# Performance work log

Measured on AMD Instinct MI355X. Metric: run time of the kernel, lower is better.

The kernel has to match this reference:

```python
import jax, jax.numpy as jnp
import numpy as np

B, H, V, S = 64, 1024, 32000, 128


def setup_inputs() -> dict:
    key = jax.random.key(0)
    ks = jax.random.split(key, 16)
    s = 1.0 / np.sqrt(H)
    return {
        "prev_input": jax.random.randint(ks[0], (B,), 0, V),
        "h0": jax.random.normal(ks[1], (B, H), jnp.float32),
        "c0": jax.random.normal(ks[2], (B, H), jnp.float32),
        "encoder_outputs": jax.random.normal(ks[3], (B, H, S), jnp.float32),
        "emb": jax.random.normal(ks[4], (V, H), jnp.float32),
        "W_ih": jax.random.uniform(ks[5], (4 * H, H), jnp.float32, -s, s),
        "W_hh": jax.random.uniform(ks[6], (4 * H, H), jnp.float32, -s, s),
        "b_ih": jax.random.uniform(ks[7], (4 * H,), jnp.float32, -s, s),
        "b_hh": jax.random.uniform(ks[8], (4 * H,), jnp.float32, -s, s),
        "W1_w": jax.random.uniform(ks[9], (H, H), jnp.float32, -s, s),
        "W1_b": jax.random.uniform(ks[10], (H,), jnp.float32, -s, s),
        "W2_w": jax.random.uniform(ks[11], (H, H), jnp.float32, -s, s),
        "W2_b": jax.random.uniform(ks[12], (H,), jnp.float32, -s, s),
        "W_w": jax.random.uniform(ks[13], (V, H), jnp.float32, -s, s),
        "W_b": jax.random.uniform(ks[14], (V,), jnp.float32, -s, s),
    }


def reference(prev_input, h0, c0, encoder_outputs, emb, W_ih, W_hh, b_ih, b_hh,
              W1_w, W1_b, W2_w, W2_b, W_w, W_b):
    # Embedding lookup (dropout omitted: eval mode)
    x = emb[prev_input]  # (B, H)
    # Single LSTM step (PyTorch gate order: i, f, g, o)
    gates = x @ W_ih.T + b_ih + h0 @ W_hh.T + b_hh  # (B, 4H)
    i, f, g, o = jnp.split(gates, 4, axis=-1)
    c_new = jax.nn.sigmoid(f) * c0 + jax.nn.sigmoid(i) * jnp.tanh(g)
    h_new = jax.nn.sigmoid(o) * jnp.tanh(c_new)  # (B, H)
    # Bahdanau-style dot attention over encoder_outputs (B, H, S)
    alpha = jax.nn.softmax(jnp.einsum('bh,bhs->bs', h_new, encoder_outputs), axis=-1)
    t = jnp.einsum('bs,bhs->bh', alpha, encoder_outputs)  # (B, H)
    # MLP classifier head
    h_att = jnp.tanh(h_new @ W1_w.T + W1_b + t @ W2_w.T + W2_b)
    y = h_att @ W_w.T + W_b  # (B, V)
    pred = jax.nn.log_softmax(y, axis=-1)
    return (pred, h_new, c_new)
```

## Files before the change

kernel.cpp:

```cpp
#include <hip/hip_runtime.h>
#include <hip/hip_bf16.h>
#include <cstdint>
#include <cstddef>

#define B_ 64
#define H_ 1024
#define V_ 32000
#define S_ 128

#define WS_GATES   0
#define WS_SCORE   524288
#define WS_HATTP   589824
#define WS_Y       851968
#define WS_BF      2899968

#define OUT_H      2048000
#define OUT_C      2113536

typedef __attribute__((ext_vector_type(8))) short bf16x8;
typedef __attribute__((ext_vector_type(4))) float f32x4;

__device__ __forceinline__ void bsplit(float x, unsigned short& hi, unsigned short& lo) {
  const unsigned int xb = __float_as_uint(x);
  hi = (unsigned short)(xb >> 16);
  const float r = x - __uint_as_float(xb & 0xFFFF0000u);
  lo = (unsigned short)(__float_as_uint(r) >> 16);
}

__global__ __launch_bounds__(256) void prep_split(
    const int* __restrict__ prev, const float* __restrict__ emb,
    const float* __restrict__ h0,
    unsigned short* __restrict__ xhi, unsigned short* __restrict__ xlo,
    unsigned short* __restrict__ hhi, unsigned short* __restrict__ hlo)
{
  const int b = blockIdx.x;
  const int k4 = threadIdx.x * 4;
  const float4 xv = *reinterpret_cast<const float4*>(emb + (size_t)prev[b] * H_ + k4);
  const float4 hv = *reinterpret_cast<const float4*>(h0 + (size_t)b * H_ + k4);
  ushort4 a, c, d, e;
  bsplit(xv.x, a.x, c.x); bsplit(xv.y, a.y, c.y);
  bsplit(xv.z, a.z, c.z); bsplit(xv.w, a.w, c.w);
  bsplit(hv.x, d.x, e.x); bsplit(hv.y, d.y, e.y);
  bsplit(hv.z, d.z, e.z); bsplit(hv.w, d.w, e.w);
  const size_t o = (size_t)b * H_ + k4;
  *reinterpret_cast<ushort4*>(xhi + o) = a;
  *reinterpret_cast<ushort4*>(xlo + o) = c;
  *reinterpret_cast<ushort4*>(hhi + o) = d;
  *reinterpret_cast<ushort4*>(hlo + o) = e;
}

__global__ __launch_bounds__(128) void gates_mfma(
    const unsigned short* __restrict__ xhi, const unsigned short* __restrict__ xlo,
    const unsigned short* __restrict__ hhi, const unsigned short* __restrict__ hlo,
    const float* __restrict__ W_ih, const float* __restrict__ W_hh,
    float* __restrict__ gates_part)
{
  const int tid = threadIdx.x;
  const int wave = tid >> 6, lane = tid & 63;
  const int l15 = lane & 15, lk = lane >> 4;
  const int ks = blockIdx.y;
  const int n = blockIdx.x * 32 + wave * 16 + l15;
  const float* W = ks ? W_hh : W_ih;
  const unsigned short* Ah = ks ? hhi : xhi;
  const unsigned short* Al = ks ? hlo : xlo;
  const float* wp = W + (size_t)n * H_ + lk * 8;
  const unsigned short* ah_base = Ah + l15 * H_ + lk * 8;
  const unsigned short* al_base = Al + l15 * H_ + lk * 8;

  f32x4 acc[4];
  #pragma unroll
  for (int mt = 0; mt < 4; ++mt) acc[mt] = (f32x4){0.f, 0.f, 0.f, 0.f};

  #pragma unroll 2
  for (int c = 0; c < 32; ++c) {
    const int k0 = c * 32;
    const float4 wv0 = *reinterpret_cast<const float4*>(wp + k0);
    const float4 wv1 = *reinterpret_cast<const float4*>(wp + k0 + 4);
    const float wf[8] = {wv0.x, wv0.y, wv0.z, wv0.w, wv1.x, wv1.y, wv1.z, wv1.w};
    bf16x8 whi, wlo;
    #pragma unroll
    for (int e = 0; e < 8; ++e) {
      const unsigned int xb = __float_as_uint(wf[e]);
      whi[e] = (short)(xb >> 16);
      const float lof = wf[e] - __uint_as_float(xb & 0xFFFF0000u);
      wlo[e] = (short)(__float_as_uint(lof) >> 16);
    }
    #pragma unroll
    for (int mt = 0; mt < 4; ++mt) {
      const bf16x8 ah = *reinterpret_cast<const bf16x8*>(ah_base + (size_t)mt * 16 * H_ + k0);
      const bf16x8 al = *reinterpret_cast<const bf16x8*>(al_base + (size_t)mt * 16 * H_ + k0);
      acc[mt] = __builtin_amdgcn_mfma_f32_16x16x32_bf16(ah, whi, acc[mt], 0, 0, 0);
      acc[mt] = __builtin_amdgcn_mfma_f32_16x16x32_bf16(al, whi, acc[mt], 0, 0, 0);
      acc[mt] = __builtin_amdgcn_mfma_f32_16x16x32_bf16(ah, wlo, acc[mt], 0, 0, 0);
    }
  }
  #pragma unroll
  for (int mt = 0; mt < 4; ++mt)
    #pragma unroll
    for (int r = 0; r < 4; ++r)
      gates_part[((size_t)ks * 64 + mt * 16 + lk * 4 + r) * 4096 + n] = acc[mt][r];
}

__global__ __launch_bounds__(128) void lstm_scores(
    const float* __restrict__ gates_part,
    const float* __restrict__ b_ih, const float* __restrict__ b_hh,
    const float* __restrict__ c0, const float* __restrict__ enc,
    float* __restrict__ out_h, float* __restrict__ out_c,
    unsigned short* __restrict__ hnhi, unsigned short* __restrict__ hnlo,
    float* __restrict__ score_part)
{
  __shared__ float hs[128];
  const int b = blockIdx.x >> 3, hc = blockIdx.x & 7;
  const int tid = threadIdx.x;
  const int h = hc * 128 + tid;

  float gi = b_ih[h]        + b_hh[h];
  float gf = b_ih[1024 + h] + b_hh[1024 + h];
  float gg = b_ih[2048 + h] + b_hh[2048 + h];
  float go = b_ih[3072 + h] + b_hh[3072 + h];
  #pragma unroll
  for (int ks = 0; ks < 2; ++ks) {
    const float* g = gates_part + ((size_t)ks * 64 + b) * 4096;
    gi += g[h]; gf += g[1024 + h]; gg += g[2048 + h]; go += g[3072 + h];
  }
  const float si = 1.f / (1.f + expf(-gi));
  const float sf = 1.f / (1.f + expf(-gf));
  const float so = 1.f / (1.f + expf(-go));
  const float cn = sf * c0[b * H_ + h] + si * tanhf(gg);
  const float hn = so * tanhf(cn);
  out_c[b * H_ + h] = cn;
  out_h[b * H_ + h] = hn;
  unsigned short hi_, lo_;
  bsplit(hn, hi_, lo_);
  hnhi[b * H_ + h] = hi_;
  hnlo[b * H_ + h] = lo_;
  hs[tid] = hn;
  __syncthreads();

  const float* e = enc + ((size_t)b * H_ + hc * 128) * S_ + tid;
  float acc = 0.f;
  #pragma unroll 8
  for (int j = 0; j < 128; ++j) acc += hs[j] * e[(size_t)j * S_];
  score_part[((size_t)hc * 64 + b) * S_ + tid] = acc;
}

__global__ __launch_bounds__(256) void attn_ctx(
    const float* __restrict__ score_part, const float* __restrict__ enc,
    unsigned short* __restrict__ thi, unsigned short* __restrict__ tlo)
{
  __shared__ __align__(16) float al[128];
  __shared__ float red[4];
  const int b = blockIdx.x >> 3, hg = blockIdx.x & 7;
  const int tid = threadIdx.x;

  float sc = 0.f;
  if (tid < 128) {
    #pragma unroll
    for (int ks = 0; ks < 8; ++ks) sc += score_part[((size_t)ks * 64 + b) * S_ + tid];
  }
  float v = (tid < 128) ? sc : -3.4e38f;
  #pragma unroll
  for (int off = 32; off; off >>= 1) v = fmaxf(v, __shfl_xor(v, off));
  if (tid == 0)  red[0] = v;
  if (tid == 64) red[1] = v;
  __syncthreads();
  const float mx = fmaxf(red[0], red[1]);
  const float ex = (tid < 128) ? expf(sc - mx) : 0.f;
  float sv = ex;
  #pragma unroll
  for (int off = 32; off; off >>= 1) sv += __shfl_xor(sv, off);
  if (tid == 0)  red[2] = sv;
  if (tid == 64) red[3] = sv;
  __syncthreads();
  const float inv = 1.f / (red[2] + red[3]);
  if (tid < 128) al[tid] = ex * inv;
  __syncthreads();

  const int wave = tid >> 6, lane = tid & 63;
  const int hoff = lane >> 5, s4 = (lane & 31) * 4;
  const float4 av = *reinterpret_cast<const float4*>(&al[s4]);
  const int hbase = hg * 128 + wave * 32;
  #pragma unroll 4
  for (int r = 0; r < 16; ++r) {
    const int h = hbase + r * 2 + hoff;
    const float4 ev = *reinterpret_cast<const float4*>(enc + ((size_t)b * H_ + h) * S_ + s4);
    float acc = ev.x * av.x + ev.y * av.y + ev.z * av.z + ev.w * av.w;
    #pragma unroll
    for (int off = 16; off; off >>= 1) acc += __shfl_xor(acc, off);
    if ((lane & 31) == 0) {
      unsigned short hi_, lo_;
      bsplit(acc, hi_, lo_);
      thi[b * H_ + h] = hi_;
      tlo[b * H_ + h] = lo_;
    }
  }
}

__global__ __launch_bounds__(128) void hatt_mfma(
    const unsigned short* __restrict__ hnhi, const unsigned short* __restrict__ hnlo,
    const unsigned short* __restrict__ thi, const unsigned short* __restrict__ tlo,
    const float* __restrict__ W1, const float* __restrict__ W2,
    float* __restrict__ hatt_part)
{
  const int tid = threadIdx.x;
  const int wave = tid >> 6, lane = tid & 63;
  const int l15 = lane & 15, lk = lane >> 4;
  const int ks = blockIdx.y;
  const int n = blockIdx.x * 32 + wave * 16 + l15;
  const int koff = (ks & 1) * 512;
  const float* W = (ks < 2) ? W1 : W2;
  const unsigned short* Ah = (ks < 2) ? hnhi : thi;
  const unsigned short* Al = (ks < 2) ? hnlo : tlo;
  const float* wp = W + (size_t)n * H_ + koff + lk * 8;
  const unsigned short* ah_base = Ah + l15 * H_ + koff + lk * 8;
  const unsigned short* al_base = Al + l15 * H_ + koff + lk * 8;

  f32x4 acc[4];
  #pragma unroll
  for (int mt = 0; mt < 4; ++mt) acc[mt] = (f32x4){0.f, 0.f, 0.f, 0.f};

  #pragma unroll 2
  for (int c = 0; c < 16; ++c) {
    const int k0 = c * 32;
    const float4 wv0 = *reinterpret_cast<const float4*>(wp + k0);
    const float4 wv1 = *reinterpret_cast<const float4*>(wp + k0 + 4);
    const float wf[8] = {wv0.x, wv0.y, wv0.z, wv0.w, wv1.x, wv1.y, wv1.z, wv1.w};
    bf16x8 whi, wlo;
    #pragma unroll
    for (int e = 0; e < 8; ++e) {
      const unsigned int xb = __float_as_uint(wf[e]);
      whi[e] = (short)(xb >> 16);
      const float lof = wf[e] - __uint_as_float(xb & 0xFFFF0000u);
      wlo[e] = (short)(__float_as_uint(lof) >> 16);
    }
    #pragma unroll
    for (int mt = 0; mt < 4; ++mt) {
      const bf16x8 ah = *reinterpret_cast<const bf16x8*>(ah_base + (size_t)mt * 16 * H_ + k0);
      const bf16x8 al = *reinterpret_cast<const bf16x8*>(al_base + (size_t)mt * 16 * H_ + k0);
      acc[mt] = __builtin_amdgcn_mfma_f32_16x16x32_bf16(ah, whi, acc[mt], 0, 0, 0);
      acc[mt] = __builtin_amdgcn_mfma_f32_16x16x32_bf16(al, whi, acc[mt], 0, 0, 0);
      acc[mt] = __builtin_amdgcn_mfma_f32_16x16x32_bf16(ah, wlo, acc[mt], 0, 0, 0);
    }
  }
  #pragma unroll
  for (int mt = 0; mt < 4; ++mt)
    #pragma unroll
    for (int r = 0; r < 4; ++r)
      hatt_part[((size_t)ks * 64 + mt * 16 + lk * 4 + r) * 1024 + n] = acc[mt][r];
}

__global__ __launch_bounds__(256) void hatt_ep(
    const float* __restrict__ hatt_part,
    const float* __restrict__ b1, const float* __restrict__ b2,
    unsigned short* __restrict__ Ahi, unsigned short* __restrict__ Alo)
{
  const int i = blockIdx.x * 256 + threadIdx.x;
  const int col = i & (H_ - 1);
  float a = b1[col] + b2[col];
  #pragma unroll
  for (int ks = 0; ks < 4; ++ks) a += hatt_part[(size_t)ks * 65536 + i];
  const float t = tanhf(a);
  unsigned short hi_, lo_;
  bsplit(t, hi_, lo_);
  Ahi[i] = hi_;
  Alo[i] = lo_;
}

__global__ __launch_bounds__(256, 2) void gemm_big_mfma(
    const unsigned short* __restrict__ Ahi, const unsigned short* __restrict__ Alo,
    const float* __restrict__ W, const float* __restrict__ bias,
    float* __restrict__ y)
{
  const int tid = threadIdx.x;
  const int wave = tid >> 6, lane = tid & 63;
  const int l15 = lane & 15, lk = lane >> 4;
  const int n = blockIdx.x * 64 + wave * 16 + l15;
  const float* wp = W + (size_t)n * H_ + lk * 8;
  const unsigned short* ah_base = Ahi + l15 * H_ + lk * 8;
  const unsigned short* al_base = Alo + l15 * H_ + lk * 8;

  f32x4 acc[4];
  #pragma unroll
  for (int mt = 0; mt < 4; ++mt) acc[mt] = (f32x4){0.f, 0.f, 0.f, 0.f};

  #pragma unroll 4
  for (int ks = 0; ks < 32; ++ks) {
    const int k0 = ks * 32;
    const float4 wv0 = *reinterpret_cast<const float4*>(wp + k0);
    const float4 wv1 = *reinterpret_cast<const float4*>(wp + k0 + 4);
    const float wf[8] = {wv0.x, wv0.y, wv0.z, wv0.w, wv1.x, wv1.y, wv1.z, wv1.w};
    bf16x8 whi, wlo;
    #pragma unroll
    for (int e = 0; e < 8; ++e) {
      const unsigned int xb = __float_as_uint(wf[e]);
      whi[e] = (short)(xb >> 16);
      const float lof = wf[e] - __uint_as_float(xb & 0xFFFF0000u);
      wlo[e] = (short)(__float_as_uint(lof) >> 16);
    }
    #pragma unroll
    for (int mt = 0; mt < 4; ++mt) {
      const bf16x8 ah = *reinterpret_cast<const bf16x8*>(ah_base + (size_t)mt * 16 * H_ + k0);
      const bf16x8 al = *reinterpret_cast<const bf16x8*>(al_base + (size_t)mt * 16 * H_ + k0);
      acc[mt] = __builtin_amdgcn_mfma_f32_16x16x32_bf16(ah, whi, acc[mt], 0, 0, 0);
      acc[mt] = __builtin_amdgcn_mfma_f32_16x16x32_bf16(al, whi, acc[mt], 0, 0, 0);
      acc[mt] = __builtin_amdgcn_mfma_f32_16x16x32_bf16(ah, wlo, acc[mt], 0, 0, 0);
    }
  }
  const float bn = bias[n];
  #pragma unroll
  for (int mt = 0; mt < 4; ++mt)
    #pragma unroll
    for (int r = 0; r < 4; ++r)
      y[(size_t)(mt * 16 + lk * 4 + r) * V_ + n] = acc[mt][r] + bn;
}

__global__ __launch_bounds__(1024) void lse_pred(
    const float* __restrict__ y, float* __restrict__ pred)
{
  __shared__ float red[16];
  __shared__ float bc;
  const int b = blockIdx.x, tid = threadIdx.x;
  const float* yr = y + (size_t)b * V_;

  float m = -3.4e38f;
  for (int i = tid; i < V_; i += 1024) m = fmaxf(m, yr[i]);
  #pragma unroll
  for (int off = 32; off; off >>= 1) m = fmaxf(m, __shfl_xor(m, off));
  if ((tid & 63) == 0) red[tid >> 6] = m;
  __syncthreads();
  if (tid == 0) {
    float mx = red[0];
    #pragma unroll
    for (int w = 1; w < 16; ++w) mx = fmaxf(mx, red[w]);
    bc = mx;
  }
  __syncthreads();
  const float mx = bc;
  float s = 0.f;
  for (int i = tid; i < V_; i += 1024) s += expf(yr[i] - mx);
  #pragma unroll
  for (int off = 32; off; off >>= 1) s += __shfl_xor(s, off);
  if ((tid & 63) == 0) red[tid >> 6] = s;
  __syncthreads();
  if (tid == 0) {
    float tot = 0.f;
    #pragma unroll
    for (int w = 0; w < 16; ++w) tot += red[w];
    bc = mx + logf(tot);
  }
  __syncthreads();
  const float lse = bc;
  float* pr = pred + (size_t)b * V_;
  for (int i = tid; i < V_; i += 1024) pr[i] = yr[i] - lse;
}

extern "C" void kernel_launch(void* const* d_in, const int* in_sizes, int n_in,
                              void* d_out, int out_size, void* d_ws, size_t ws_size,
                              hipStream_t stream)
{
  const int*   prev = (const int*)  d_in[0];
  const float* h0   = (const float*)d_in[1];
  const float* c0   = (const float*)d_in[2];
  const float* enc  = (const float*)d_in[3];
  const float* emb  = (const float*)d_in[4];
  const float* W_ih = (const float*)d_in[5];
  const float* W_hh = (const float*)d_in[6];
  const float* b_ih = (const float*)d_in[7];
  const float* b_hh = (const float*)d_in[8];
  const float* W1_w = (const float*)d_in[9];
  const float* W1_b = (const float*)d_in[10];
  const float* W2_w = (const float*)d_in[11];
  const float* W2_b = (const float*)d_in[12];
  const float* W_w  = (const float*)d_in[13];
  const float* W_b  = (const float*)d_in[14];

  float* outp  = (float*)d_out;
  float* pred  = outp;
  float* h_new = outp + OUT_H;
  float* c_new = outp + OUT_C;

  float* ws         = (float*)d_ws;
  float* gates_part = ws + WS_GATES;
  float* score_part = ws + WS_SCORE;
  float* hatt_part  = ws + WS_HATTP;
  float* y          = ws + WS_Y;
  unsigned short* us = (unsigned short*)(ws + WS_BF);
  unsigned short* xhi  = us;
  unsigned short* xlo  = us + 65536;
  unsigned short* h0hi = us + 131072;
  unsigned short* h0lo = us + 196608;
  unsigned short* hnhi = us + 262144;
  unsigned short* hnlo = us + 327680;
  unsigned short* thi  = us + 393216;
  unsigned short* tlo  = us + 458752;
  unsigned short* Ahi  = us + 524288;
  unsigned short* Alo  = us + 589824;

  prep_split<<<64, 256, 0, stream>>>(prev, emb, h0, xhi, xlo, h0hi, h0lo);
  gates_mfma<<<dim3(128, 2), 128, 0, stream>>>(
      xhi, xlo, h0hi, h0lo, W_ih, W_hh, gates_part);
  lstm_scores<<<512, 128, 0, stream>>>(
      gates_part, b_ih, b_hh, c0, enc, h_new, c_new, hnhi, hnlo, score_part);
  attn_ctx<<<512, 256, 0, stream>>>(score_part, enc, thi, tlo);
  hatt_mfma<<<dim3(32, 4), 128, 0, stream>>>(
      hnhi, hnlo, thi, tlo, W1_w, W2_w, hatt_part);
  hatt_ep<<<256, 256, 0, stream>>>(hatt_part, W1_b, W2_b, Ahi, Alo);
  gemm_big_mfma<<<500, 256, 0, stream>>>(Ahi, Alo, W_w, W_b, y);
  lse_pred<<<64, 1024, 0, stream>>>(y, pred);
}
```

Measured before the change: 419.6 us.

## Split-K all GEMMs, software-pipeline weight loads, split LSTM/scores and two-pass log-softmax

```diff
diff --git a/kernel.cpp b/kernel.cpp
--- a/kernel.cpp
+++ b/kernel.cpp
@@ -9,10 +9,11 @@
 #define S_ 128
 
 #define WS_GATES   0
-#define WS_SCORE   524288
-#define WS_HATTP   589824
-#define WS_Y       851968
-#define WS_BF      2899968
+#define WS_SCORE   2097152
+#define WS_HATTP   2228224
+#define WS_YP      2752512
+#define WS_STATS   6848512
+#define WS_BF      6849536
 
 #define OUT_H      2048000
 #define OUT_C      2113536
@@ -25,6 +26,48 @@
   hi = (unsigned short)(xb >> 16);
   const float r = x - __uint_as_float(xb & 0xFFFF0000u);
   lo = (unsigned short)(__float_as_uint(r) >> 16);
+}
+
+template<int NITER>
+__device__ __forceinline__ void mfma_panel(
+    const float* __restrict__ wp,
+    const unsigned short* __restrict__ ah_base,
+    const unsigned short* __restrict__ al_base,
+    f32x4 acc[4])
+{
+  float4 w0 = *reinterpret_cast<const float4*>(wp);
+  float4 w1 = *reinterpret_cast<const float4*>(wp + 4);
+  #pragma unroll
+  for (int c = 0; c < NITER; ++c) {
+    const int k0 = c * 32;
+    float4 nw0, nw1;
+    if (c + 1 < NITER) {
+      nw0 = *reinterpret_cast<const float4*>(wp + k0 + 32);
+      nw1 = *reinterpret_cast<const float4*>(wp + k0 + 36);
+    }
+    bf16x8 ah[4], al[4];
+    #pragma unroll
+    for (int mt = 0; mt < 4; ++mt) {
+      ah[mt] = *reinterpret_cast<const bf16x8*>(ah_base + (size_t)mt * 16 * H_ + k0);
+      al[mt] = *reinterpret_cast<const bf16x8*>(al_base + (size_t)mt * 16 * H_ + k0);
+    }
+    const float wf[8] = {w0.x, w0.y, w0.z, w0.w, w1.x, w1.y, w1.z, w1.w};
+    bf16x8 whi, wlo;
+    #pragma unroll
+    for (int e = 0; e < 8; ++e) {
+      const unsigned int xb = __float_as_uint(wf[e]);
+      whi[e] = (short)(xb >> 16);
+      const float lof = wf[e] - __uint_as_float(xb & 0xFFFF0000u);
+      wlo[e] = (short)(__float_as_uint(lof) >> 16);
+    }
+    #pragma unroll
+    for (int mt = 0; mt < 4; ++mt) {
+      acc[mt] = __builtin_amdgcn_mfma_f32_16x16x32_bf16(ah[mt], whi, acc[mt], 0, 0, 0);
+      acc[mt] = __builtin_amdgcn_mfma_f32_16x16x32_bf16(al[mt], whi, acc[mt], 0, 0, 0);
+      acc[mt] = __builtin_amdgcn_mfma_f32_16x16x32_bf16(ah[mt], wlo, acc[mt], 0, 0, 0);
+    }
+    if (c + 1 < NITER) { w0 = nw0; w1 = nw1; }
+  }
 }
 
 __global__ __launch_bounds__(256) void prep_split(
@@ -49,7 +92,7 @@
   *reinterpret_cast<ushort4*>(hlo + o) = e;
 }
 
-__global__ __launch_bounds__(128) void gates_mfma(
+__global__ __launch_bounds__(256, 4) void gates_mfma(
     const unsigned short* __restrict__ xhi, const unsigned short* __restrict__ xlo,
     const unsigned short* __restrict__ hhi, const unsigned short* __restrict__ hlo,
     const float* __restrict__ W_ih, const float* __restrict__ W_hh,
@@ -59,41 +102,18 @@
   const int wave = tid >> 6, lane = tid & 63;
   const int l15 = lane & 15, lk = lane >> 4;
   const int ks = blockIdx.y;
-  const int n = blockIdx.x * 32 + wave * 16 + l15;
-  const float* W = ks ? W_hh : W_ih;
-  const unsigned short* Ah = ks ? hhi : xhi;
-  const unsigned short* Al = ks ? hlo : xlo;
-  const float* wp = W + (size_t)n * H_ + lk * 8;
-  const unsigned short* ah_base = Ah + l15 * H_ + lk * 8;
-  const unsigned short* al_base = Al + l15 * H_ + lk * 8;
+  const int mat = ks >> 2, koff = (ks & 3) * 256;
+  const int n = blockIdx.x * 64 + wave * 16 + l15;
+  const float* W = mat ? W_hh : W_ih;
+  const unsigned short* Ah = mat ? hhi : xhi;
+  const unsigned short* Al = mat ? hlo : xlo;
 
   f32x4 acc[4];
   #pragma unroll
   for (int mt = 0; mt < 4; ++mt) acc[mt] = (f32x4){0.f, 0.f, 0.f, 0.f};
-
-  #pragma unroll 2
-  for (int c = 0; c < 32; ++c) {
-    const int k0 = c * 32;
-    const float4 wv0 = *reinterpret_cast<const float4*>(wp + k0);
-    const float4 wv1 = *reinterpret_cast<const float4*>(wp + k0 + 4);
-    const float wf[8] = {wv0.x, wv0.y, wv0.z, wv0.w, wv1.x, wv1.y, wv1.z, wv1.w};
-    bf16x8 whi, wlo;
-    #pragma unroll
-    for (int e = 0; e < 8; ++e) {
-      const unsigned int xb = __float_as_uint(wf[e]);
-      whi[e] = (short)(xb >> 16);
-      const float lof = wf[e] - __uint_as_float(xb & 0xFFFF0000u);
-      wlo[e] = (short)(__float_as_uint(lof) >> 16);
-    }
-    #pragma unroll
-    for (int mt = 0; mt < 4; ++mt) {
-      const bf16x8 ah = *reinterpret_cast<const bf16x8*>(ah_base + (size_t)mt * 16 * H_ + k0);
-      const bf16x8 al = *reinterpret_cast<const bf16x8*>(al_base + (size_t)mt * 16 * H_ + k0);
-      acc[mt] = __builtin_amdgcn_mfma_f32_16x16x32_bf16(ah, whi, acc[mt], 0, 0, 0);
-      acc[mt] = __builtin_amdgcn_mfma_f32_16x16x32_bf16(al, whi, acc[mt], 0, 0, 0);
-      acc[mt] = __builtin_amdgcn_mfma_f32_16x16x32_bf16(ah, wlo, acc[mt], 0, 0, 0);
-    }
-  }
+  mfma_panel<8>(W + (size_t)n * H_ + koff + lk * 8,
+                Ah + l15 * H_ + koff + lk * 8,
+                Al + l15 * H_ + koff + lk * 8, acc);
   #pragma unroll
   for (int mt = 0; mt < 4; ++mt)
     #pragma unroll
@@ -101,46 +121,51 @@
       gates_part[((size_t)ks * 64 + mt * 16 + lk * 4 + r) * 4096 + n] = acc[mt][r];
 }
 
-__global__ __launch_bounds__(128) void lstm_scores(
+__global__ __launch_bounds__(256) void k_lstm(
     const float* __restrict__ gates_part,
     const float* __restrict__ b_ih, const float* __restrict__ b_hh,
-    const float* __restrict__ c0, const float* __restrict__ enc,
+    const float* __restrict__ c0,
     float* __restrict__ out_h, float* __restrict__ out_c,
-    unsigned short* __restrict__ hnhi, unsigned short* __restrict__ hnlo,
-    float* __restrict__ score_part)
-{
-  __shared__ float hs[128];
-  const int b = blockIdx.x >> 3, hc = blockIdx.x & 7;
-  const int tid = threadIdx.x;
-  const int h = hc * 128 + tid;
-
+    unsigned short* __restrict__ hnhi, unsigned short* __restrict__ hnlo)
+{
+  const int i = blockIdx.x * 256 + threadIdx.x;
+  const int h = i & (H_ - 1);
   float gi = b_ih[h]        + b_hh[h];
   float gf = b_ih[1024 + h] + b_hh[1024 + h];
   float gg = b_ih[2048 + h] + b_hh[2048 + h];
   float go = b_ih[3072 + h] + b_hh[3072 + h];
-  #pragma unroll
-  for (int ks = 0; ks < 2; ++ks) {
+  const int b = i >> 10;
+  #pragma unroll
+  for (int ks = 0; ks < 8; ++ks) {
     const float* g = gates_part + ((size_t)ks * 64 + b) * 4096;
     gi += g[h]; gf += g[1024 + h]; gg += g[2048 + h]; go += g[3072 + h];
   }
   const float si = 1.f / (1.f + expf(-gi));
   const float sf = 1.f / (1.f + expf(-gf));
   const float so = 1.f / (1.f + expf(-go));
-  const float cn = sf * c0[b * H_ + h] + si * tanhf(gg);
+  const float cn = sf * c0[i] + si * tanhf(gg);
   const float hn = so * tanhf(cn);
-  out_c[b * H_ + h] = cn;
-  out_h[b * H_ + h] = hn;
+  out_c[i] = cn;
+  out_h[i] = hn;
   unsigned short hi_, lo_;
   bsplit(hn, hi_, lo_);
-  hnhi[b * H_ + h] = hi_;
-  hnlo[b * H_ + h] = lo_;
-  hs[tid] = hn;
+  hnhi[i] = hi_;
+  hnlo[i] = lo_;
+}
+
+__global__ __launch_bounds__(128) void k_scores(
+    const float* __restrict__ h_new, const float* __restrict__ enc,
+    float* __restrict__ score_part)
+{
+  __shared__ float hs[64];
+  const int b = blockIdx.x >> 4, hc = blockIdx.x & 15;
+  const int tid = threadIdx.x;
+  if (tid < 64) hs[tid] = h_new[b * H_ + hc * 64 + tid];
   __syncthreads();
-
-  const float* e = enc + ((size_t)b * H_ + hc * 128) * S_ + tid;
+  const float* e = enc + ((size_t)b * H_ + hc * 64) * S_ + tid;
   float acc = 0.f;
   #pragma unroll 8
-  for (int j = 0; j < 128; ++j) acc += hs[j] * e[(size_t)j * S_];
+  for (int j = 0; j < 64; ++j) acc += hs[j] * e[(size_t)j * S_];
   score_part[((size_t)hc * 64 + b) * S_ + tid] = acc;
 }
 
@@ -156,7 +181,7 @@
   float sc = 0.f;
   if (tid < 128) {
     #pragma unroll
-    for (int ks = 0; ks < 8; ++ks) sc += score_part[((size_t)ks * 64 + b) * S_ + tid];
+    for (int ks = 0; ks < 16; ++ks) sc += score_part[((size_t)ks * 64 + b) * S_ + tid];
   }
   float v = (tid < 128) ? sc : -3.4e38f;
   #pragma unroll
@@ -180,7 +205,7 @@
   const int hoff = lane >> 5, s4 = (lane & 31) * 4;
   const float4 av = *reinterpret_cast<const float4*>(&al[s4]);
   const int hbase = hg * 128 + wave * 32;
-  #pragma unroll 4
+  #pragma unroll 8
   for (int r = 0; r < 16; ++r) {
     const int h = hbase + r * 2 + hoff;
     const float4 ev = *reinterpret_cast<const float4*>(enc + ((size_t)b * H_ + h) * S_ + s4);
@@ -196,7 +221,7 @@
   }
 }
 
-__global__ __launch_bounds__(128) void hatt_mfma(
+__global__ __launch_bounds__(256, 4) void hatt_mfma(
     const unsigned short* __restrict__ hnhi, const unsigned short* __restrict__ hnlo,
     const unsigned short* __restrict__ thi, const unsigned short* __restrict__ tlo,
     const float* __restrict__ W1, const float* __restrict__ W2,
@@ -206,42 +231,18 @@
   const int wave = tid >> 6, lane = tid & 63;
   const int l15 = lane & 15, lk = lane >> 4;
   const int ks = blockIdx.y;
-  const int n = blockIdx.x * 32 + wave * 16 + l15;
-  const int koff = (ks & 1) * 512;
-  const float* W = (ks < 2) ? W1 : W2;
-  const unsigned short* Ah = (ks < 2) ? hnhi : thi;
-  const unsigned short* Al = (ks < 2) ? hnlo : tlo;
-  const float* wp = W + (size_t)n * H_ + koff + lk * 8;
-  const unsigned short* ah_base = Ah + l15 * H_ + koff + lk * 8;
-  const unsigned short* al_base = Al + l15 * H_ + koff + lk * 8;
+  const int mat = ks >> 2, koff = (ks & 3) * 256;
+  const int n = blockIdx.x * 64 + wave * 16 + l15;
+  const float* W = mat ? W2 : W1;
+  const unsigned short* Ah = mat ? thi : hnhi;
+  const unsigned short* Al = mat ? tlo : hnlo;
 
   f32x4 acc[4];
   #pragma unroll
   for (int mt = 0; mt < 4; ++mt) acc[mt] = (f32x4){0.f, 0.f, 0.f, 0.f};
-
-  #pragma unroll 2
-  for (int c = 0; c < 16; ++c) {
-    const int k0 = c * 32;
-    const float4 wv0 = *reinterpret_cast<const float4*>(wp + k0);
-    const float4 wv1 = *reinterpret_cast<const float4*>(wp + k0 + 4);
-    const float wf[8] = {wv0.x, wv0.y, wv0.z, wv0.w, wv1.x, wv1.y, wv1.z, wv1.w};
-    bf16x8 whi, wlo;
-    #pragma unroll
-    for (int e = 0; e < 8; ++e) {
-      const unsigned int xb = __float_as_uint(wf[e]);
-      whi[e] = (short)(xb >> 16);
-      const float lof = wf[e] - __uint_as_float(xb & 0xFFFF0000u);
-      wlo[e] = (short)(__float_as_uint(lof) >> 16);
-    }
-    #pragma unroll
-    for (int mt = 0; mt < 4; ++mt) {
-      const bf16x8 ah = *reinterpret_cast<const bf16x8*>(ah_base + (size_t)mt * 16 * H_ + k0);
-      const bf16x8 al = *reinterpret_cast<const bf16x8*>(al_base + (size_t)mt * 16 * H_ + k0);
-      acc[mt] = __builtin_amdgcn_mfma_f32_16x16x32_bf16(ah, whi, acc[mt], 0, 0, 0);
-      acc[mt] = __builtin_amdgcn_mfma_f32_16x16x32_bf16(al, whi, acc[mt], 0, 0, 0);
-      acc[mt] = __builtin_amdgcn_mfma_f32_16x16x32_bf16(ah, wlo, acc[mt], 0, 0, 0);
-    }
-  }
+  mfma_panel<8>(W + (size_t)n * H_ + koff + lk * 8,
+                Ah + l15 * H_ + koff + lk * 8,
+                Al + l15 * H_ + koff + lk * 8, acc);
   #pragma unroll
   for (int mt = 0; mt < 4; ++mt)
     #pragma unroll
@@ -258,7 +259,7 @@
   const int col = i & (H_ - 1);
   float a = b1[col] + b2[col];
   #pragma unroll
-  for (int ks = 0; ks < 4; ++ks) a += hatt_part[(size_t)ks * 65536 + i];
+  for (int ks = 0; ks < 8; ++ks) a += hatt_part[(size_t)ks * 65536 + i];
   const float t = tanhf(a);
   unsigned short hi_, lo_;
   bsplit(t, hi_, lo_);
@@ -266,92 +267,101 @@
   Alo[i] = lo_;
 }
 
-__global__ __launch_bounds__(256, 2) void gemm_big_mfma(
+__global__ __launch_bounds__(256, 4) void gemm_big_mfma(
     const unsigned short* __restrict__ Ahi, const unsigned short* __restrict__ Alo,
-    const float* __restrict__ W, const float* __restrict__ bias,
-    float* __restrict__ y)
+    const float* __restrict__ W, float* __restrict__ ypart)
 {
   const int tid = threadIdx.x;
   const int wave = tid >> 6, lane = tid & 63;
   const int l15 = lane & 15, lk = lane >> 4;
+  const int ks = blockIdx.y, koff = ks * 512;
   const int n = blockIdx.x * 64 + wave * 16 + l15;
-  const float* wp = W + (size_t)n * H_ + lk * 8;
-  const unsigned short* ah_base = Ahi + l15 * H_ + lk * 8;
-  const unsigned short* al_base = Alo + l15 * H_ + lk * 8;
 
   f32x4 acc[4];
   #pragma unroll
   for (int mt = 0; mt < 4; ++mt) acc[mt] = (f32x4){0.f, 0.f, 0.f, 0.f};
-
-  #pragma unroll 4
-  for (int ks = 0; ks < 32; ++ks) {
-    const int k0 = ks * 32;
-    const float4 wv0 = *reinterpret_cast<const float4*>(wp + k0);
-    const float4 wv1 = *reinterpret_cast<const float4*>(wp + k0 + 4);
-    const float wf[8] = {wv0.x, wv0.y, wv0.z, wv0.w, wv1.x, wv1.y, wv1.z, wv1.w};
-    bf16x8 whi, wlo;
-    #pragma unroll
-    for (int e = 0; e < 8; ++e) {
-      const unsigned int xb = __float_as_uint(wf[e]);
-      whi[e] = (short)(xb >> 16);
-      const float lof = wf[e] - __uint_as_float(xb & 0xFFFF0000u);
-      wlo[e] = (short)(__float_as_uint(lof) >> 16);
-    }
-    #pragma unroll
-    for (int mt = 0; mt < 4; ++mt) {
-      const bf16x8 ah = *reinterpret_cast<const bf16x8*>(ah_base + (size_t)mt * 16 * H_ + k0);
-      const bf16x8 al = *reinterpret_cast<const bf16x8*>(al_base + (size_t)mt * 16 * H_ + k0);
-      acc[mt] = __builtin_amdgcn_mfma_f32_16x16x32_bf16(ah, whi, acc[mt], 0, 0, 0);
-      acc[mt] = __builtin_amdgcn_mfma_f32_16x16x32_bf16(al, whi, acc[mt], 0, 0, 0);
-      acc[mt] = __builtin_amdgcn_mfma_f32_16x16x32_bf16(ah, wlo, acc[mt], 0, 0, 0);
-    }
-  }
-  const float bn = bias[n];
+  mfma_panel<16>(W + (size_t)n * H_ + koff + lk * 8,
+                 Ahi + l15 * H_ + koff + lk * 8,
+                 Alo + l15 * H_ + koff + lk * 8, acc);
+  float* yp = ypart + (size_t)ks * 64 * V_;
   #pragma unroll
   for (int mt = 0; mt < 4; ++mt)
     #pragma unroll
     for (int r = 0; r < 4; ++r)
-      y[(size_t)(mt * 16 + lk * 4 + r) * V_ + n] = acc[mt][r] + bn;
-}
-
-__global__ __launch_bounds__(1024) void lse_pred(
-    const float* __restrict__ y, float* __restrict__ pred)
-{
-  __shared__ float red[16];
-  __shared__ float bc;
-  const int b = blockIdx.x, tid = threadIdx.x;
-  const float* yr = y + (size_t)b * V_;
-
+      yp[(size_t)(mt * 16 + lk * 4 + r) * V_ + n] = acc[mt][r];
+}
+
+__global__ __launch_bounds__(256) void lse1(
+    const float* __restrict__ yp, const float* __restrict__ bias,
+    float* __restrict__ stats)
+{
+  __shared__ float sm[4][2];
+  const int b = blockIdx.x >> 3, ch = blockIdx.x & 7;
+  const int tid = threadIdx.x;
+  const float* p0 = yp + (size_t)b * V_ + ch * 4000;
+  const float* p1 = p0 + (size_t)64 * V_;
+  const float* bs = bias + ch * 4000;
+
+  float v[16];
   float m = -3.4e38f;
-  for (int i = tid; i < V_; i += 1024) m = fmaxf(m, yr[i]);
-  #pragma unroll
-  for (int off = 32; off; off >>= 1) m = fmaxf(m, __shfl_xor(m, off));
-  if ((tid & 63) == 0) red[tid >> 6] = m;
+  #pragma unroll
+  for (int j = 0; j < 16; ++j) {
+    const int c = tid + j * 256;
+    if (c < 4000) {
+      v[j] = p0[c] + p1[c] + bs[c];
+      m = fmaxf(m, v[j]);
+    }
+  }
+  float s = 0.f;
+  #pragma unroll
+  for (int j = 0; j < 16; ++j) {
+    const int c = tid + j * 256;
+    if (c < 4000) s += expf(v[j] - m);
+  }
+  #pragma unroll
+  for (int off = 32; off; off >>= 1) {
+    const float m2 = __shfl_xor(m, off);
+    const float s2 = __shfl_xor(s, off);
+    const float M = fmaxf(m, m2);
+    s = s * expf(m - M) + s2 * expf(m2 - M);
+    m = M;
+  }
+  if ((tid & 63) == 0) { sm[tid >> 6][0] = m; sm[tid >> 6][1] = s; }
   __syncthreads();
   if (tid == 0) {
-    float mx = red[0];
-    #pragma unroll
-    for (int w = 1; w < 16; ++w) mx = fmaxf(mx, red[w]);
-    bc = mx;
-  }
-  __syncthreads();
-  const float mx = bc;
-  float s = 0.f;
-  for (int i = tid; i < V_; i += 1024) s += expf(yr[i] - mx);
-  #pragma unroll
-  for (int off = 32; off; off >>= 1) s += __shfl_xor(s, off);
-  if ((tid & 63) == 0) red[tid >> 6] = s;
-  __syncthreads();
-  if (tid == 0) {
-    float tot = 0.f;
-    #pragma unroll
-    for (int w = 0; w < 16; ++w) tot += red[w];
-    bc = mx + logf(tot);
-  }
-  __syncthreads();
-  const float lse = bc;
-  float* pr = pred + (size_t)b * V_;
-  for (int i = tid; i < V_; i += 1024) pr[i] = yr[i] - lse;
+    float M = fmaxf(fmaxf(sm[0][0], sm[1][0]), fmaxf(sm[2][0], sm[3][0]));
+    float S = 0.f;
+    #pragma unroll
+    for (int w = 0; w < 4; ++w) S += sm[w][1] * expf(sm[w][0] - M);
+    stats[(b * 8 + ch) * 2]     = M;
+    stats[(b * 8 + ch) * 2 + 1] = S;
+  }
+}
+
+__global__ __launch_bounds__(256) void lse2(
+    const float* __restrict__ yp, const float* __restrict__ bias,
+    const float* __restrict__ stats, float* __restrict__ pred)
+{
+  const int b = blockIdx.x >> 3, ch = blockIdx.x & 7;
+  const int tid = threadIdx.x;
+  float M = -3.4e38f;
+  #pragma unroll
+  for (int i = 0; i < 8; ++i) M = fmaxf(M, stats[(b * 8 + i) * 2]);
+  float S = 0.f;
+  #pragma unroll
+  for (int i = 0; i < 8; ++i)
+    S += stats[(b * 8 + i) * 2 + 1] * expf(stats[(b * 8 + i) * 2] - M);
+  const float lse = M + logf(S);
+
+  const float* p0 = yp + (size_t)b * V_ + ch * 4000;
+  const float* p1 = p0 + (size_t)64 * V_;
+  const float* bs = bias + ch * 4000;
+  float* pr = pred + (size_t)b * V_ + ch * 4000;
+  #pragma unroll
+  for (int j = 0; j < 16; ++j) {
+    const int c = tid + j * 256;
+    if (c < 4000) pr[c] = p0[c] + p1[c] + bs[c] - lse;
+  }
 }
 
 extern "C" void kernel_launch(void* const* d_in, const int* in_sizes, int n_in,
@@ -383,7 +393,8 @@
   float* gates_part = ws + WS_GATES;
   float* score_part = ws + WS_SCORE;
   float* hatt_part  = ws + WS_HATTP;
-  float* y          = ws + WS_Y;
+  float* ypart      = ws + WS_YP;
+  float* stats      = ws + WS_STATS;
   unsigned short* us = (unsigned short*)(ws + WS_BF);
   unsigned short* xhi  = us;
   unsigned short* xlo  = us + 65536;
@@ -397,14 +408,16 @@
   unsigned short* Alo  = us + 589824;
 
   prep_split<<<64, 256, 0, stream>>>(prev, emb, h0, xhi, xlo, h0hi, h0lo);
-  gates_mfma<<<dim3(128, 2), 128, 0, stream>>>(
+  gates_mfma<<<dim3(64, 8), 256, 0, stream>>>(
       xhi, xlo, h0hi, h0lo, W_ih, W_hh, gates_part);
-  lstm_scores<<<512, 128, 0, stream>>>(
-      gates_part, b_ih, b_hh, c0, enc, h_new, c_new, hnhi, hnlo, score_part);
+  k_lstm<<<256, 256, 0, stream>>>(
+      gates_part, b_ih, b_hh, c0, h_new, c_new, hnhi, hnlo);
+  k_scores<<<1024, 128, 0, stream>>>(h_new, enc, score_part);
   attn_ctx<<<512, 256, 0, stream>>>(score_part, enc, thi, tlo);
-  hatt_mfma<<<dim3(32, 4), 128, 0, stream>>>(
+  hatt_mfma<<<dim3(16, 8), 256, 0, stream>>>(
       hnhi, hnlo, thi, tlo, W1_w, W2_w, hatt_part);
   hatt_ep<<<256, 256, 0, stream>>>(hatt_part, W1_b, W2_b, Ahi, Alo);
-  gemm_big_mfma<<<500, 256, 0, stream>>>(Ahi, Alo, W_w, W_b, y);
-  lse_pred<<<64, 1024, 0, stream>>>(y, pred);
-}
+  gemm_big_mfma<<<dim3(500, 2), 256, 0, stream>>>(Ahi, Alo, W_w, ypart);
+  lse1<<<512, 256, 0, stream>>>(ypart, W_b, stats);
+  lse2<<<512, 256, 0, stream>>>(ypart, W_b, stats, pred);
+}
```

After: 399.4 us. 4.8% less time.
